# Kernel optimization log

Hardware: AMD Instinct MI355X
Metric: run time of the kernel (lower is better)

Reference implementation:

```python
import jax, jax.numpy as jnp
import numpy as np

B, N, F_IN, H, MH, STEPS = 8192, 9, 15, 128, 256, 4
E_PER = 16
MASK_IDX = jnp.arange(8)  # mask = [True]*8 + [False]


def setup_inputs() -> dict:
    key = jax.random.key(0)
    ks = jax.random.split(key, 24)
    s = 0.05
    inp = {
        "obs": jax.random.normal(ks[0], (B, 135), jnp.float32),
        "edges": jax.random.randint(ks[1], (B, 2, E_PER), 0, N, jnp.int32),
        "enc_W": jax.random.normal(ks[2], (F_IN, H), jnp.float32) * s,
        "enc_b": jax.random.normal(ks[3], (H,), jnp.float32) * s,
        "msg_W1": jax.random.normal(ks[4], (STEPS, 2 * H, MH), jnp.float32) * s,
        "msg_b1": jax.random.normal(ks[5], (STEPS, MH), jnp.float32) * s,
        "msg_W2": jax.random.normal(ks[6], (STEPS, MH, MH), jnp.float32) * s,
        "msg_b2": jax.random.normal(ks[7], (STEPS, MH), jnp.float32) * s,
        "msg_W3": jax.random.normal(ks[8], (STEPS, MH, H), jnp.float32) * s,
        "msg_b3": jax.random.normal(ks[9], (STEPS, H), jnp.float32) * s,
        "gru_Wi": jax.random.normal(ks[10], (STEPS, H, 3 * H), jnp.float32) * s,
        "gru_Wh": jax.random.normal(ks[11], (STEPS, H, 3 * H), jnp.float32) * s,
        "gru_bi": jax.random.normal(ks[12], (STEPS, 3 * H), jnp.float32) * s,
        "gru_bh": jax.random.normal(ks[13], (STEPS, 3 * H), jnp.float32) * s,
        "dec_W1": jax.random.normal(ks[14], (H, MH), jnp.float32) * s,
        "dec_b1": jax.random.normal(ks[15], (MH,), jnp.float32) * s,
        "dec_W2": jax.random.normal(ks[16], (MH, MH), jnp.float32) * s,
        "dec_b2": jax.random.normal(ks[17], (MH,), jnp.float32) * s,
        "dec_W3": jax.random.normal(ks[18], (MH, 1), jnp.float32) * s,
        "dec_b3": jax.random.normal(ks[19], (1,), jnp.float32) * s,
    }
    return inp


def reference(obs, edges, enc_W, enc_b, msg_W1, msg_b1, msg_W2, msg_b2,
              msg_W3, msg_b3, gru_Wi, gru_Wh, gru_bi, gru_bh,
              dec_W1, dec_b1, dec_W2, dec_b2, dec_W3, dec_b3):
    BN = B * N
    x = obs.reshape(BN, F_IN)                       # [B*N, 15]
    x = jnp.tanh(x @ enc_W + enc_b)                 # encoder -> [B*N, H]

    # flatten per-graph edges into a global edge list, then add self-loops
    offsets = (jnp.arange(B, dtype=jnp.int32) * N)[:, None, None]
    eg = edges + offsets                            # [B, 2, 16]
    loops = jnp.arange(BN, dtype=jnp.int32)
    src = jnp.concatenate([eg[:, 0, :].reshape(-1), loops])  # x_j (source)
    dst = jnp.concatenate([eg[:, 1, :].reshape(-1), loops])  # x_i (target)
    deg = jax.ops.segment_sum(jnp.ones_like(dst, dtype=x.dtype), dst,
                              num_segments=BN)      # >=1 due to self-loops

    for s in range(STEPS):
        m = jnp.concatenate([x[dst], x[src]], axis=-1)       # [E, 2H]
        m = jnp.tanh(m @ msg_W1[s] + msg_b1[s])
        m = jnp.tanh(m @ msg_W2[s] + msg_b2[s])
        m = m @ msg_W3[s] + msg_b3[s]                        # [E, H]
        aggr = jax.ops.segment_sum(m, dst, num_segments=BN) / deg[:, None]
        # GRUCell(input=aggr, hidden=x), PyTorch gate order (r, z, n)
        gi = aggr @ gru_Wi[s] + gru_bi[s]
        gh = x @ gru_Wh[s] + gru_bh[s]
        ir, iz, inn = jnp.split(gi, 3, axis=-1)
        hr, hz, hn = jnp.split(gh, 3, axis=-1)
        r = jax.nn.sigmoid(ir + hr)
        z = jax.nn.sigmoid(iz + hz)
        n = jnp.tanh(inn + r * hn)
        x = (1.0 - z) * n + z * x

    d = jnp.tanh(x @ dec_W1 + dec_b1)
    d = jnp.tanh(d @ dec_W2 + dec_b2)
    d = d @ dec_W3 + dec_b3                                  # [B*N, 1]
    out = d.reshape(B, N)
    return out[:, MASK_IDX]                                  # [B, 8]
```

## Files before the change

kernel.cpp:

```cpp
#include <hip/hip_runtime.h>
#include <hip/hip_bf16.h>
#include <math.h>

#define BGR   8192
#define NND   9
#define BN    73728
#define NE    131072
#define H     128
#define MH    256
#define FIN   15

typedef __bf16 bf16_t;
typedef bf16_t bf16x8 __attribute__((ext_vector_type(8)));
typedef float  f32x4  __attribute__((ext_vector_type(4)));
typedef float  f32x16 __attribute__((ext_vector_type(16)));

__device__ __forceinline__ unsigned short f2bf(float f) {
    unsigned int u = __float_as_uint(f);
    u += 0x7fff + ((u >> 16) & 1);
    return (unsigned short)(u >> 16);
}
__device__ __forceinline__ unsigned int pkbf(float a, float b) {
    union { __hip_bfloat162 h; unsigned int u; } un;
    un.h = __float22bfloat162_rn(make_float2(a, b));
    return un.u;
}
__device__ __forceinline__ bf16x8 as_frag(int4 v) {
    union { int4 i; bf16x8 f; } u; u.i = v; return u.f;
}
__device__ __forceinline__ float fast_tanh(float v) {
    float e = __expf(2.0f * v);
    return 1.0f - __fdividef(2.0f, e + 1.0f);
}
__device__ __forceinline__ int sw16(int m, int k) {
    return m * 256 + ((((k >> 3) ^ (m & 15)) << 3) | (k & 7));
}
__device__ __forceinline__ int swp(int m, int k) {
    return m * 128 + ((((k >> 3) ^ (m & 15)) << 3) | (k & 7));
}
__device__ __forceinline__ int sw_off(int m, int k) {
    return m * 256 + ((((k >> 3) ^ (m & 7)) << 3) | (k & 7));
}

__global__ void deg_kernel(const int* __restrict__ edges, float* __restrict__ inv_deg) {
    int g = blockIdx.x * 256 + threadIdx.x;
    if (g >= BGR) return;
    int cnt[NND];
#pragma unroll
    for (int n = 0; n < NND; ++n) cnt[n] = 1;
    for (int j = 0; j < 16; ++j) {
        int d = edges[g * 32 + 16 + j];
#pragma unroll
        for (int n = 0; n < NND; ++n) cnt[n] += (d == n) ? 1 : 0;
    }
#pragma unroll
    for (int n = 0; n < NND; ++n) inv_deg[g * NND + n] = 1.0f / (float)cnt[n];
}

__global__ void enc_kernel(const float* __restrict__ obs, const float* __restrict__ W,
                           const float* __restrict__ b, float* __restrict__ x) {
    int tid = blockIdx.x * 256 + threadIdx.x;
    int i = tid >> 7, h = tid & 127;
    float acc = b[h];
#pragma unroll
    for (int k = 0; k < FIN; ++k) acc += obs[i * FIN + k] * W[k * H + h];
    x[i * H + h] = tanhf(acc);
}

__global__ void wt_kernel(const float* __restrict__ W1, const float* __restrict__ W2,
                          const float* __restrict__ W3, const float* __restrict__ Wi,
                          const float* __restrict__ Wh, const float* __restrict__ dW1,
                          const float* __restrict__ dW2, unsigned short* __restrict__ out) {
    int idx = blockIdx.x * 256 + threadIdx.x;
    float v;
    if (idx < 262144) {
        int s = idx >> 16, r = idx & 65535, n = r >> 8, k = r & 255;
        v = W1[(s << 16) + (k << 8) + n];
    } else if (idx < 524288) {
        int i2 = idx - 262144;
        int s = i2 >> 16, r = i2 & 65535, n = r >> 8, k = r & 255;
        v = W2[(s << 16) + (k << 8) + n];
    } else if (idx < 655360) {
        int i3 = idx - 524288;
        int s = i3 >> 15, r = i3 & 32767, n = r >> 8, k = r & 255;
        v = W3[(s << 15) + (k << 7) + n];
    } else if (idx < 1179648) {
        int i4 = idx - 655360;
        int s = i4 >> 17, rr = i4 & 131071;
        int p = rr >> 8, k = rr & 255;
        int w = p >> 6, rem = p & 63;
        int gate = rem >> 4, c = rem & 15;
        int h = w * 16 + c;
        const int sb = s * 49152;
        if (gate == 0)      v = (k < 128) ? Wi[sb + k * 384 + h]       : Wh[sb + (k - 128) * 384 + h];
        else if (gate == 1) v = (k < 128) ? Wi[sb + k * 384 + 128 + h] : Wh[sb + (k - 128) * 384 + 128 + h];
        else if (gate == 2) v = (k < 128) ? Wi[sb + k * 384 + 256 + h] : 0.f;
        else                v = (k < 128) ? 0.f                        : Wh[sb + (k - 128) * 384 + 256 + h];
    } else if (idx < 1212416) {
        int i5 = idx - 1179648;
        int n = i5 >> 7, k = i5 & 127;
        v = dW1[k * 256 + n];
    } else if (idx < 1277952) {
        int i6 = idx - 1212416;
        int n = i6 >> 8, k = i6 & 255;
        v = dW2[k * 256 + n];
    } else {
        int i7 = idx - 1277952;
        int s = i7 >> 16, rr = i7 & 65535;
        int p = rr >> 7, k = rr & 127;
        int w = p >> 6, rem = p & 63;
        int side = rem >> 5, c = rem & 31;
        int n = w * 32 + c;
        v = W1[(s << 16) + ((k + side * 128) << 8) + n];
    }
    out[idx] = f2bf(v);
}

__global__ __launch_bounds__(512, 4) void proj_mfma(
        const float* __restrict__ x, const unsigned short* __restrict__ W1P,
        const float* __restrict__ b1,
        const unsigned short* __restrict__ W2T, const float* __restrict__ b2,
        const unsigned short* __restrict__ W3T,
        unsigned short* __restrict__ P, float* __restrict__ aggr) {
    __shared__ unsigned short lbuf[64 * 128];
    __shared__ unsigned short abuf[64 * 256];
    const int t = threadIdx.x;
    const int n0 = blockIdx.x * 64;
    const int wv = t >> 6, ln = t & 63, l31 = ln & 31, lh = ln >> 5;

    {
        const int m = t >> 3, q = t & 7;
        const float* xs = x + (size_t)(n0 + m) * H + q * 16;
#pragma unroll
        for (int i = 0; i < 4; ++i) {
            float4 v = *(const float4*)(xs + i * 4);
            uint2 o; o.x = pkbf(v.x, v.y); o.y = pkbf(v.z, v.w);
            *(uint2*)(lbuf + swp(m, q * 16 + i * 4)) = o;
        }
    }
    __syncthreads();

    {
        f32x16 au[2], av[2];
#pragma unroll
        for (int a = 0; a < 2; ++a)
#pragma unroll
            for (int i = 0; i < 16; ++i) { au[a][i] = 0.f; av[a][i] = 0.f; }
        const unsigned short* wpu = W1P + (size_t)(wv * 64 + l31) * 128 + lh * 8;
        const unsigned short* wpv = W1P + (size_t)(wv * 64 + 32 + l31) * 128 + lh * 8;
#pragma unroll
        for (int ks = 0; ks < 8; ++ks) {
            const int kk = ks * 16 + lh * 8;
            bf16x8 a0 = as_frag(*(const int4*)(lbuf + swp(l31, kk)));
            bf16x8 a1 = as_frag(*(const int4*)(lbuf + swp(32 + l31, kk)));
            bf16x8 wu = as_frag(*(const int4*)(wpu + ks * 16));
            bf16x8 wvv = as_frag(*(const int4*)(wpv + ks * 16));
            au[0] = __builtin_amdgcn_mfma_f32_32x32x16_bf16(a0, wu, au[0], 0, 0, 0);
            au[1] = __builtin_amdgcn_mfma_f32_32x32x16_bf16(a1, wu, au[1], 0, 0, 0);
            av[0] = __builtin_amdgcn_mfma_f32_32x32x16_bf16(a0, wvv, av[0], 0, 0, 0);
            av[1] = __builtin_amdgcn_mfma_f32_32x32x16_bf16(a1, wvv, av[1], 0, 0, 0);
        }
        const int n = wv * 32 + l31;
        const float bias = b1[n];
#pragma unroll
        for (int mt = 0; mt < 2; ++mt)
#pragma unroll
            for (int reg = 0; reg < 16; ++reg) {
                const int mrow = mt * 32 + (reg & 3) + ((reg >> 2) << 3) + (lh << 2);
                const size_t node = n0 + mrow;
                P[node * 512 + n]       = f2bf(au[mt][reg]);
                P[node * 512 + 256 + n] = f2bf(av[mt][reg]);
                abuf[sw16(mrow, n)] = f2bf(fast_tanh(au[mt][reg] + av[mt][reg] + bias));
            }
    }
    __syncthreads();

    {
        f32x16 acc0, acc1;
#pragma unroll
        for (int i = 0; i < 16; ++i) { acc0[i] = 0.f; acc1[i] = 0.f; }
        const unsigned short* wp = W2T + (size_t)(wv * 32 + l31) * 256 + lh * 8;
#pragma unroll
        for (int ks = 0; ks < 16; ++ks) {
            const int kk = ks * 16 + lh * 8;
            bf16x8 a0 = as_frag(*(const int4*)(abuf + sw16(l31, kk)));
            bf16x8 a1 = as_frag(*(const int4*)(abuf + sw16(32 + l31, kk)));
            bf16x8 bw = as_frag(*(const int4*)(wp + ks * 16));
            acc0 = __builtin_amdgcn_mfma_f32_32x32x16_bf16(a0, bw, acc0, 0, 0, 0);
            acc1 = __builtin_amdgcn_mfma_f32_32x32x16_bf16(a1, bw, acc1, 0, 0, 0);
        }
        __syncthreads();
        const int n = wv * 32 + l31;
        const float bias = b2[n];
#pragma unroll
        for (int reg = 0; reg < 16; ++reg) {
            const int mrow = (reg & 3) + ((reg >> 2) << 3) + (lh << 2);
            abuf[sw16(mrow, n)]      = f2bf(fast_tanh(acc0[reg] + bias));
            abuf[sw16(32 + mrow, n)] = f2bf(fast_tanh(acc1[reg] + bias));
        }
    }
    __syncthreads();

    {
        const int mt = wv & 1, nq = wv >> 1;
        const int n = nq * 32 + l31;
        f32x16 acc;
#pragma unroll
        for (int i = 0; i < 16; ++i) acc[i] = 0.f;
        const unsigned short* wp = W3T + (size_t)n * 256 + lh * 8;
#pragma unroll
        for (int ks = 0; ks < 16; ++ks) {
            const int kk = ks * 16 + lh * 8;
            bf16x8 a = as_frag(*(const int4*)(abuf + sw16(mt * 32 + l31, kk)));
            bf16x8 bw = as_frag(*(const int4*)(wp + ks * 16));
            acc = __builtin_amdgcn_mfma_f32_32x32x16_bf16(a, bw, acc, 0, 0, 0);
        }
#pragma unroll
        for (int reg = 0; reg < 16; ++reg) {
            const int m = mt * 32 + (reg & 3) + ((reg >> 2) << 3) + (lh << 2);
            aggr[(size_t)(n0 + m) * H + n] = acc[reg];
        }
    }
}

__global__ __launch_bounds__(512, 4) void msg_mfma(
        const unsigned short* __restrict__ P, const int* __restrict__ edges,
        const float* __restrict__ b1,
        const unsigned short* __restrict__ W2T, const float* __restrict__ b2,
        const unsigned short* __restrict__ W3T,
        float* __restrict__ aggr) {
    __shared__ unsigned short bufA[64 * 256];
    __shared__ unsigned short bufB[64 * 256];
    __shared__ unsigned char sdstL[64];
    const int t  = threadIdx.x;
    const int e0 = blockIdx.x * 64;
    const int wv = t >> 6;
    const int ln = t & 63;
    const int l31 = ln & 31;
    const int lh  = ln >> 5;

    if (t < 64) {
        const int eg = e0 + t;
        sdstL[t] = (unsigned char)(((eg >> 4) & 3) * NND + edges[(eg >> 4) * 32 + 16 + (eg & 15)]);
    }
    {
        const int row = t >> 3;
        const int c0  = (t & 7) * 32;
        const int eg  = e0 + row;
        const int g = eg >> 4, j = eg & 15;
        const int sn = g * NND + edges[g * 32 + j];
        const int dn = g * NND + edges[g * 32 + 16 + j];
        const unsigned short* up = P + (size_t)dn * 512 + c0;
        const unsigned short* vp = P + (size_t)sn * 512 + 256 + c0;
#pragma unroll
        for (int i = 0; i < 4; ++i) {
            const uint4 uu = *(const uint4*)(up + i * 8);
            const uint4 vv = *(const uint4*)(vp + i * 8);
            const unsigned int ua[4] = {uu.x, uu.y, uu.z, uu.w};
            const unsigned int va[4] = {vv.x, vv.y, vv.z, vv.w};
            unsigned int op[4];
#pragma unroll
            for (int j2 = 0; j2 < 4; ++j2) {
                const float2 bb = *(const float2*)(b1 + c0 + i * 8 + j2 * 2);
                const float s0 = fast_tanh(__uint_as_float(ua[j2] << 16) +
                                           __uint_as_float(va[j2] << 16) + bb.x);
                const float s1 = fast_tanh(__uint_as_float(ua[j2] & 0xffff0000u) +
                                           __uint_as_float(va[j2] & 0xffff0000u) + bb.y);
                op[j2] = pkbf(s0, s1);
            }
            *(uint4*)(bufA + sw16(row, c0 + i * 8)) = make_uint4(op[0], op[1], op[2], op[3]);
        }
    }
    __syncthreads();

    {
        f32x16 acc0, acc1;
#pragma unroll
        for (int i = 0; i < 16; ++i) { acc0[i] = 0.f; acc1[i] = 0.f; }
        const unsigned short* wp = W2T + (size_t)(wv * 32 + l31) * 256 + lh * 8;
#pragma unroll
        for (int ks = 0; ks < 16; ++ks) {
            const int kk = ks * 16 + lh * 8;
            bf16x8 a0 = as_frag(*(const int4*)(bufA + sw16(l31, kk)));
            bf16x8 a1 = as_frag(*(const int4*)(bufA + sw16(32 + l31, kk)));
            bf16x8 bw = as_frag(*(const int4*)(wp + ks * 16));
            acc0 = __builtin_amdgcn_mfma_f32_32x32x16_bf16(a0, bw, acc0, 0, 0, 0);
            acc1 = __builtin_amdgcn_mfma_f32_32x32x16_bf16(a1, bw, acc1, 0, 0, 0);
        }
        const int n = wv * 32 + l31;
        const float bias = b2[n];
#pragma unroll
        for (int reg = 0; reg < 16; ++reg) {
            const int mrow = (reg & 3) + ((reg >> 2) << 3) + (lh << 2);
            bufB[sw16(mrow, n)]      = f2bf(fast_tanh(acc0[reg] + bias));
            bufB[sw16(32 + mrow, n)] = f2bf(fast_tanh(acc1[reg] + bias));
        }
    }
    __syncthreads();

    float* aL = (float*)bufA;
#pragma unroll
    for (int i = 0; i < 9; ++i) aL[i * 512 + t] = 0.f;
    __syncthreads();

    {
        const int mt = wv & 1, nq = wv >> 1;
        const int n = nq * 32 + l31;
        f32x16 acc;
#pragma unroll
        for (int i = 0; i < 16; ++i) acc[i] = 0.f;
        const unsigned short* wp = W3T + (size_t)n * 256 + lh * 8;
#pragma unroll
        for (int ks = 0; ks < 16; ++ks) {
            const int kk = ks * 16 + lh * 8;
            bf16x8 a = as_frag(*(const int4*)(bufB + sw16(mt * 32 + l31, kk)));
            bf16x8 bw = as_frag(*(const int4*)(wp + ks * 16));
            acc = __builtin_amdgcn_mfma_f32_32x32x16_bf16(a, bw, acc, 0, 0, 0);
        }
#pragma unroll
        for (int reg = 0; reg < 16; ++reg) {
            const int m = mt * 32 + (reg & 3) + ((reg >> 2) << 3) + (lh << 2);
            atomicAdd(&aL[(int)sdstL[m] * 128 + n], acc[reg]);
        }
    }
    __syncthreads();

    {
        float* gp = aggr + (size_t)blockIdx.x * 36 * 128;
#pragma unroll
        for (int i = 0; i < 9; ++i) {
            const int idx = i * 512 + t;
            gp[idx] += aL[idx];
        }
    }
}

__global__ __launch_bounds__(512, 4) void gru_mfma(
        float* __restrict__ x, float* __restrict__ aggr, const float* __restrict__ inv_deg,
        const unsigned short* __restrict__ WG, const float* __restrict__ b3m,
        const float* __restrict__ bi, const float* __restrict__ bh) {
    __shared__ unsigned short bufA[64 * 256];
    const int t = threadIdx.x;
    const int n0 = blockIdx.x * 64;
    const int wv = t >> 6, ln = t & 63, lrow = ln & 15, lq = ln >> 4;

    {
        const int m = t >> 3;
        const int q = t & 7;
        const int k0 = q * 32;
        const int node = n0 + m;
        if (q < 4) {
            const float scale = inv_deg[node];
            const float* src = aggr + (size_t)node * H + k0;
#pragma unroll
            for (int i = 0; i < 8; ++i) {
                float4 v = *(const float4*)(src + i * 4);
                const float4 bb = *(const float4*)(b3m + k0 + i * 4);
                v.x = v.x * scale + bb.x; v.y = v.y * scale + bb.y;
                v.z = v.z * scale + bb.z; v.w = v.w * scale + bb.w;
                uint2 o; o.x = pkbf(v.x, v.y); o.y = pkbf(v.z, v.w);
                *(uint2*)(bufA + sw_off(m, k0 + i * 4)) = o;
            }
        } else {
            const float* src = x + (size_t)node * H + (k0 - 128);
#pragma unroll
            for (int i = 0; i < 8; ++i) {
                float4 v = *(const float4*)(src + i * 4);
                uint2 o; o.x = pkbf(v.x, v.y); o.y = pkbf(v.z, v.w);
                *(uint2*)(bufA + sw_off(m, k0 + i * 4)) = o;
            }
        }
    }
    __syncthreads();

    const f32x4 zero = {0.f, 0.f, 0.f, 0.f};
    f32x4 acc[4][4];
#pragma unroll
    for (int i = 0; i < 4; ++i)
#pragma unroll
        for (int j = 0; j < 4; ++j) acc[i][j] = zero;

    const unsigned short* wgp = WG + (size_t)(wv * 64 + lrow) * 256;
#pragma unroll
    for (int kq = 0; kq < 8; ++kq) {
        const int ko = kq * 32 + lq * 8;
        bf16x8 af[4], bfr[4];
#pragma unroll
        for (int tm = 0; tm < 4; ++tm)
            af[tm] = as_frag(*(const int4*)(bufA + sw_off(tm * 16 + lrow, ko)));
#pragma unroll
        for (int g = 0; g < 4; ++g)
            bfr[g] = as_frag(*(const int4*)(wgp + (size_t)g * 16 * 256 + ko));
#pragma unroll
        for (int tm = 0; tm < 4; ++tm)
#pragma unroll
            for (int g = 0; g < 4; ++g)
                acc[tm][g] = __builtin_amdgcn_mfma_f32_16x16x32_bf16(af[tm], bfr[g], acc[tm][g], 0, 0, 0);
    }

    {
        const int h = wv * 16 + lrow;
        const float b_r = bi[h] + bh[h];
        const float b_z = bi[128 + h] + bh[128 + h];
        const float b_n = bi[256 + h];
        const float b_h = bh[256 + h];
#pragma unroll
        for (int tm = 0; tm < 4; ++tm) {
#pragma unroll
            for (int r = 0; r < 4; ++r) {
                const int node = n0 + tm * 16 + lq * 4 + r;
                const float irhr = acc[tm][0][r] + b_r;
                const float izhz = acc[tm][1][r] + b_z;
                const float inn  = acc[tm][2][r] + b_n;
                const float hn   = acc[tm][3][r] + b_h;
                const float rg = 1.f / (1.f + expf(-irhr));
                const float zg = 1.f / (1.f + expf(-izhz));
                const float ng = tanhf(inn + rg * hn);
                const float xo = x[(size_t)node * H + h];
                x[(size_t)node * H + h] = (1.f - zg) * ng + zg * xo;
            }
        }
    }
}

__global__ __launch_bounds__(256, 4) void dec_mfma(
        const float* __restrict__ x,
        const unsigned short* __restrict__ W1T, const float* __restrict__ b1,
        const unsigned short* __restrict__ W2T, const float* __restrict__ b2,
        const float* __restrict__ W3, const float* __restrict__ b3,
        float* __restrict__ out) {
    __shared__ unsigned short buf[64 * 256];
    const int t = threadIdx.x;
    const int id0 = blockIdx.x * 64;
    const int wv = t >> 6, ln = t & 63, lrow = ln & 15, lq = ln >> 4;
    const int nbase = wv * 64;

    {
        const int m = t >> 2, q = t & 3;
        const int id = id0 + m;
        const int node = (id >> 3) * NND + (id & 7);
        const float* src = x + (size_t)node * H + q * 32;
#pragma unroll
        for (int i = 0; i < 8; ++i) {
            float4 v = *(const float4*)(src + i * 4);
            uint2 o; o.x = pkbf(v.x, v.y); o.y = pkbf(v.z, v.w);
            *(uint2*)(buf + sw_off(m, q * 32 + i * 4)) = o;
        }
    }
    __syncthreads();

    const f32x4 zero = {0.f, 0.f, 0.f, 0.f};

    {
        f32x4 acc[4][4];
#pragma unroll
        for (int i = 0; i < 4; ++i)
#pragma unroll
            for (int j = 0; j < 4; ++j) acc[i][j] = zero;
#pragma unroll
        for (int kq = 0; kq < 4; ++kq) {
            const int ko = kq * 32 + lq * 8;
            bf16x8 af[4], bfr[4];
#pragma unroll
            for (int tm = 0; tm < 4; ++tm)
                af[tm] = as_frag(*(const int4*)(buf + sw_off(tm * 16 + lrow, ko)));
#pragma unroll
            for (int tn = 0; tn < 4; ++tn)
                bfr[tn] = as_frag(*(const int4*)(W1T + (size_t)(nbase + tn * 16 + lrow) * 128 + ko));
#pragma unroll
            for (int tm = 0; tm < 4; ++tm)
#pragma unroll
                for (int tn = 0; tn < 4; ++tn)
                    acc[tm][tn] = __builtin_amdgcn_mfma_f32_16x16x32_bf16(af[tm], bfr[tn], acc[tm][tn], 0, 0, 0);
        }
        __syncthreads();
#pragma unroll
        for (int tn = 0; tn < 4; ++tn) {
            const int n = nbase + tn * 16 + lrow;
            const float bias = b1[n];
#pragma unroll
            for (int tm = 0; tm < 4; ++tm)
#pragma unroll
                for (int r = 0; r < 4; ++r) {
                    const int m = tm * 16 + lq * 4 + r;
                    buf[sw_off(m, n)] = f2bf(fast_tanh(acc[tm][tn][r] + bias));
                }
        }
    }
    __syncthreads();

    {
        f32x4 acc[4][4];
#pragma unroll
        for (int i = 0; i < 4; ++i)
#pragma unroll
            for (int j = 0; j < 4; ++j) acc[i][j] = zero;
#pragma unroll
        for (int kq = 0; kq < 8; ++kq) {
            const int ko = kq * 32 + lq * 8;
            bf16x8 af[4], bfr[4];
#pragma unroll
            for (int tm = 0; tm < 4; ++tm)
                af[tm] = as_frag(*(const int4*)(buf + sw_off(tm * 16 + lrow, ko)));
#pragma unroll
            for (int tn = 0; tn < 4; ++tn)
                bfr[tn] = as_frag(*(const int4*)(W2T + (size_t)(nbase + tn * 16 + lrow) * 256 + ko));
#pragma unroll
            for (int tm = 0; tm < 4; ++tm)
#pragma unroll
                for (int tn = 0; tn < 4; ++tn)
                    acc[tm][tn] = __builtin_amdgcn_mfma_f32_16x16x32_bf16(af[tm], bfr[tn], acc[tm][tn], 0, 0, 0);
        }
        __syncthreads();
#pragma unroll
        for (int tn = 0; tn < 4; ++tn) {
            const int n = nbase + tn * 16 + lrow;
            const float bias = b2[n];
#pragma unroll
            for (int tm = 0; tm < 4; ++tm)
#pragma unroll
                for (int r = 0; r < 4; ++r) {
                    const int m = tm * 16 + lq * 4 + r;
                    buf[sw_off(m, n)] = f2bf(fast_tanh(acc[tm][tn][r] + bias));
                }
        }
    }
    __syncthreads();

    {
        const int m = t >> 2, p = t & 3;
        float s = 0.f;
#pragma unroll
        for (int i = 0; i < 64; ++i) {
            const int k = p * 64 + i;
            const float a = __uint_as_float((unsigned int)buf[sw_off(m, k)] << 16);
            s += a * W3[k];
        }
        s += __shfl_xor(s, 1);
        s += __shfl_xor(s, 2);
        if (p == 0) out[id0 + m] = s + b3[0];
    }
}

extern "C" void kernel_launch(void* const* d_in, const int* in_sizes, int n_in,
                              void* d_out, int out_size, void* d_ws, size_t ws_size,
                              hipStream_t stream) {
    const float* obs    = (const float*)d_in[0];
    const int*   edges  = (const int*)  d_in[1];
    const float* enc_W  = (const float*)d_in[2];
    const float* enc_b  = (const float*)d_in[3];
    const float* msg_W1 = (const float*)d_in[4];
    const float* msg_b1 = (const float*)d_in[5];
    const float* msg_W2 = (const float*)d_in[6];
    const float* msg_b2 = (const float*)d_in[7];
    const float* msg_W3 = (const float*)d_in[8];
    const float* msg_b3 = (const float*)d_in[9];
    const float* gru_Wi = (const float*)d_in[10];
    const float* gru_Wh = (const float*)d_in[11];
    const float* gru_bi = (const float*)d_in[12];
    const float* gru_bh = (const float*)d_in[13];
    const float* dec_W1 = (const float*)d_in[14];
    const float* dec_b1 = (const float*)d_in[15];
    const float* dec_W2 = (const float*)d_in[16];
    const float* dec_b2 = (const float*)d_in[17];
    const float* dec_W3 = (const float*)d_in[18];
    const float* dec_b3 = (const float*)d_in[19];

    float* x       = (float*)d_ws;
    float* aggr    = x + (size_t)BN * H;
    float* inv_deg = aggr + (size_t)BN * H;
    unsigned short* wbf = (unsigned short*)(inv_deg + BN);
    unsigned short* P   = wbf + 1540096;

    deg_kernel<<<(BGR + 255) / 256, 256, 0, stream>>>(edges, inv_deg);
    wt_kernel<<<1540096 / 256, 256, 0, stream>>>(msg_W1, msg_W2, msg_W3, gru_Wi, gru_Wh,
                                                 dec_W1, dec_W2, wbf);
    enc_kernel<<<BN * H / 256, 256, 0, stream>>>(obs, enc_W, enc_b, x);

    for (int s = 0; s < 4; ++s) {
        const unsigned short* W2T = wbf + 262144 + (size_t)s * 65536;
        const unsigned short* W3T = wbf + 524288 + (size_t)s * 32768;
        const unsigned short* WGs = wbf + 655360 + (size_t)s * 131072;
        const unsigned short* W1P = wbf + 1277952 + (size_t)s * 65536;
        proj_mfma<<<BN / 64, 512, 0, stream>>>(
            x, W1P, msg_b1 + (size_t)s * 256,
            W2T, msg_b2 + (size_t)s * 256, W3T, P, aggr);
        msg_mfma<<<NE / 64, 512, 0, stream>>>(
            P, edges,
            msg_b1 + (size_t)s * 256,
            W2T, msg_b2 + (size_t)s * 256,
            W3T,
            aggr);
        gru_mfma<<<BN / 64, 512, 0, stream>>>(
            x, aggr, inv_deg, WGs, msg_b3 + (size_t)s * 128,
            gru_bi + (size_t)s * 384, gru_bh + (size_t)s * 384);
    }

    dec_mfma<<<BGR * 8 / 64, 256, 0, stream>>>(
        x, wbf + 1179648, dec_b1, wbf + 1212416, dec_b2, dec_W3, dec_b3, (float*)d_out);
}
```

Baseline: 1.499 ms.

## Fuse next-step node projection into GRU kernel to drop separate proj launches

The GRU kernel now also computes the next message-passing step's per-node projection: it keeps the updated node state as bf16 in shared memory and runs the W1/W2/W3 MLP chain, writing P and the self-loop aggregate. Only the first step still launches proj_mfma separately. This avoids re-reading x from global memory and removes three kernel launches. The cost is 16KB more shared memory per block and higher register pressure in the fused kernel, which may reduce occupancy.

```diff
diff --git a/kernel.cpp b/kernel.cpp
--- a/kernel.cpp
+++ b/kernel.cpp
@@ -335,14 +335,20 @@
     }
 }
 
-__global__ __launch_bounds__(512, 4) void gru_mfma(
+__global__ __launch_bounds__(512, 4) void grup_mfma(
         float* __restrict__ x, float* __restrict__ aggr, const float* __restrict__ inv_deg,
         const unsigned short* __restrict__ WG, const float* __restrict__ b3m,
-        const float* __restrict__ bi, const float* __restrict__ bh) {
+        const float* __restrict__ bi, const float* __restrict__ bh,
+        const unsigned short* __restrict__ W1Pn, const float* __restrict__ b1n,
+        const unsigned short* __restrict__ W2Tn, const float* __restrict__ b2n,
+        const unsigned short* __restrict__ W3Tn,
+        unsigned short* __restrict__ P, int do_next) {
     __shared__ unsigned short bufA[64 * 256];
+    __shared__ unsigned short xbL[64 * 128];
     const int t = threadIdx.x;
     const int n0 = blockIdx.x * 64;
     const int wv = t >> 6, ln = t & 63, lrow = ln & 15, lq = ln >> 4;
+    const int l31 = ln & 31, lh = ln >> 5;
 
     {
         const int m = t >> 3;
@@ -373,32 +379,32 @@
     }
     __syncthreads();
 
-    const f32x4 zero = {0.f, 0.f, 0.f, 0.f};
-    f32x4 acc[4][4];
-#pragma unroll
-    for (int i = 0; i < 4; ++i)
-#pragma unroll
-        for (int j = 0; j < 4; ++j) acc[i][j] = zero;
-
-    const unsigned short* wgp = WG + (size_t)(wv * 64 + lrow) * 256;
-#pragma unroll
-    for (int kq = 0; kq < 8; ++kq) {
-        const int ko = kq * 32 + lq * 8;
-        bf16x8 af[4], bfr[4];
-#pragma unroll
-        for (int tm = 0; tm < 4; ++tm)
-            af[tm] = as_frag(*(const int4*)(bufA + sw_off(tm * 16 + lrow, ko)));
-#pragma unroll
-        for (int g = 0; g < 4; ++g)
-            bfr[g] = as_frag(*(const int4*)(wgp + (size_t)g * 16 * 256 + ko));
-#pragma unroll
-        for (int tm = 0; tm < 4; ++tm)
+    {
+        const f32x4 zero = {0.f, 0.f, 0.f, 0.f};
+        f32x4 acc[4][4];
+#pragma unroll
+        for (int i = 0; i < 4; ++i)
+#pragma unroll
+            for (int j = 0; j < 4; ++j) acc[i][j] = zero;
+
+        const unsigned short* wgp = WG + (size_t)(wv * 64 + lrow) * 256;
+#pragma unroll
+        for (int kq = 0; kq < 8; ++kq) {
+            const int ko = kq * 32 + lq * 8;
+            bf16x8 af[4], bfr[4];
+#pragma unroll
+            for (int tm = 0; tm < 4; ++tm)
+                af[tm] = as_frag(*(const int4*)(bufA + sw_off(tm * 16 + lrow, ko)));
 #pragma unroll
             for (int g = 0; g < 4; ++g)
-                acc[tm][g] = __builtin_amdgcn_mfma_f32_16x16x32_bf16(af[tm], bfr[g], acc[tm][g], 0, 0, 0);
-    }
-
-    {
+                bfr[g] = as_frag(*(const int4*)(wgp + (size_t)g * 16 * 256 + ko));
+#pragma unroll
+            for (int tm = 0; tm < 4; ++tm)
+#pragma unroll
+                for (int g = 0; g < 4; ++g)
+                    acc[tm][g] = __builtin_amdgcn_mfma_f32_16x16x32_bf16(af[tm], bfr[g], acc[tm][g], 0, 0, 0);
+        }
+
         const int h = wv * 16 + lrow;
         const float b_r = bi[h] + bh[h];
         const float b_z = bi[128 + h] + bh[128 + h];
@@ -408,7 +414,8 @@
         for (int tm = 0; tm < 4; ++tm) {
 #pragma unroll
             for (int r = 0; r < 4; ++r) {
-                const int node = n0 + tm * 16 + lq * 4 + r;
+                const int ml = tm * 16 + lq * 4 + r;
+                const int node = n0 + ml;
                 const float irhr = acc[tm][0][r] + b_r;
                 const float izhz = acc[tm][1][r] + b_z;
                 const float inn  = acc[tm][2][r] + b_n;
@@ -417,8 +424,94 @@
                 const float zg = 1.f / (1.f + expf(-izhz));
                 const float ng = tanhf(inn + rg * hn);
                 const float xo = x[(size_t)node * H + h];
-                x[(size_t)node * H + h] = (1.f - zg) * ng + zg * xo;
+                const float xn = (1.f - zg) * ng + zg * xo;
+                x[(size_t)node * H + h] = xn;
+                xbL[swp(ml, h)] = f2bf(xn);
             }
+        }
+    }
+    if (!do_next) return;
+    __syncthreads();
+
+    {
+        f32x16 au[2], av[2];
+#pragma unroll
+        for (int a = 0; a < 2; ++a)
+#pragma unroll
+            for (int i = 0; i < 16; ++i) { au[a][i] = 0.f; av[a][i] = 0.f; }
+        const unsigned short* wpu = W1Pn + (size_t)(wv * 64 + l31) * 128 + lh * 8;
+        const unsigned short* wpv = W1Pn + (size_t)(wv * 64 + 32 + l31) * 128 + lh * 8;
+#pragma unroll
+        for (int ks = 0; ks < 8; ++ks) {
+            const int kk = ks * 16 + lh * 8;
+            bf16x8 a0 = as_frag(*(const int4*)(xbL + swp(l31, kk)));
+            bf16x8 a1 = as_frag(*(const int4*)(xbL + swp(32 + l31, kk)));
+            bf16x8 wu = as_frag(*(const int4*)(wpu + ks * 16));
+            bf16x8 wvv = as_frag(*(const int4*)(wpv + ks * 16));
+            au[0] = __builtin_amdgcn_mfma_f32_32x32x16_bf16(a0, wu, au[0], 0, 0, 0);
+            au[1] = __builtin_amdgcn_mfma_f32_32x32x16_bf16(a1, wu, au[1], 0, 0, 0);
+            av[0] = __builtin_amdgcn_mfma_f32_32x32x16_bf16(a0, wvv, av[0], 0, 0, 0);
+            av[1] = __builtin_amdgcn_mfma_f32_32x32x16_bf16(a1, wvv, av[1], 0, 0, 0);
+        }
+        const int n = wv * 32 + l31;
+        const float bias = b1n[n];
+#pragma unroll
+        for (int mt = 0; mt < 2; ++mt)
+#pragma unroll
+            for (int reg = 0; reg < 16; ++reg) {
+                const int mrow = mt * 32 + (reg & 3) + ((reg >> 2) << 3) + (lh << 2);
+                const size_t node = n0 + mrow;
+                P[node * 512 + n]       = f2bf(au[mt][reg]);
+                P[node * 512 + 256 + n] = f2bf(av[mt][reg]);
+                bufA[sw16(mrow, n)] = f2bf(fast_tanh(au[mt][reg] + av[mt][reg] + bias));
+            }
+    }
+    __syncthreads();
+
+    {
+        f32x16 acc0, acc1;
+#pragma unroll
+        for (int i = 0; i < 16; ++i) { acc0[i] = 0.f; acc1[i] = 0.f; }
+        const unsigned short* wp = W2Tn + (size_t)(wv * 32 + l31) * 256 + lh * 8;
+#pragma unroll
+        for (int ks = 0; ks < 16; ++ks) {
+            const int kk = ks * 16 + lh * 8;
+            bf16x8 a0 = as_frag(*(const int4*)(bufA + sw16(l31, kk)));
+            bf16x8 a1 = as_frag(*(const int4*)(bufA + sw16(32 + l31, kk)));
+            bf16x8 bw = as_frag(*(const int4*)(wp + ks * 16));
+            acc0 = __builtin_amdgcn_mfma_f32_32x32x16_bf16(a0, bw, acc0, 0, 0, 0);
+            acc1 = __builtin_amdgcn_mfma_f32_32x32x16_bf16(a1, bw, acc1, 0, 0, 0);
+        }
+        __syncthreads();
+        const int n = wv * 32 + l31;
+        const float bias = b2n[n];
+#pragma unroll
+        for (int reg = 0; reg < 16; ++reg) {
+            const int mrow = (reg & 3) + ((reg >> 2) << 3) + (lh << 2);
+            bufA[sw16(mrow, n)]      = f2bf(fast_tanh(acc0[reg] + bias));
+            bufA[sw16(32 + mrow, n)] = f2bf(fast_tanh(acc1[reg] + bias));
+        }
+    }
+    __syncthreads();
+
+    {
+        const int mt = wv & 1, nq = wv >> 1;
+        const int n = nq * 32 + l31;
+        f32x16 acc;
+#pragma unroll
+        for (int i = 0; i < 16; ++i) acc[i] = 0.f;
+        const unsigned short* wp = W3Tn + (size_t)n * 256 + lh * 8;
+#pragma unroll
+        for (int ks = 0; ks < 16; ++ks) {
+            const int kk = ks * 16 + lh * 8;
+            bf16x8 a = as_frag(*(const int4*)(bufA + sw16(mt * 32 + l31, kk)));
+            bf16x8 bw = as_frag(*(const int4*)(wp + ks * 16));
+            acc = __builtin_amdgcn_mfma_f32_32x32x16_bf16(a, bw, acc, 0, 0, 0);
+        }
+#pragma unroll
+        for (int reg = 0; reg < 16; ++reg) {
+            const int m = mt * 32 + (reg & 3) + ((reg >> 2) << 3) + (lh << 2);
+            aggr[(size_t)(n0 + m) * H + n] = acc[reg];
         }
     }
 }
@@ -577,23 +670,31 @@
                                                  dec_W1, dec_W2, wbf);
     enc_kernel<<<BN * H / 256, 256, 0, stream>>>(obs, enc_W, enc_b, x);
 
+    proj_mfma<<<BN / 64, 512, 0, stream>>>(
+        x, wbf + 1277952, msg_b1,
+        wbf + 262144, msg_b2, wbf + 524288, P, aggr);
+
     for (int s = 0; s < 4; ++s) {
         const unsigned short* W2T = wbf + 262144 + (size_t)s * 65536;
         const unsigned short* W3T = wbf + 524288 + (size_t)s * 32768;
         const unsigned short* WGs = wbf + 655360 + (size_t)s * 131072;
-        const unsigned short* W1P = wbf + 1277952 + (size_t)s * 65536;
-        proj_mfma<<<BN / 64, 512, 0, stream>>>(
-            x, W1P, msg_b1 + (size_t)s * 256,
-            W2T, msg_b2 + (size_t)s * 256, W3T, P, aggr);
+        const int nx = (s < 3) ? s + 1 : s;
+        const unsigned short* W1Pn = wbf + 1277952 + (size_t)nx * 65536;
+        const unsigned short* W2Tn = wbf + 262144 + (size_t)nx * 65536;
+        const unsigned short* W3Tn = wbf + 524288 + (size_t)nx * 32768;
         msg_mfma<<<NE / 64, 512, 0, stream>>>(
             P, edges,
             msg_b1 + (size_t)s * 256,
             W2T, msg_b2 + (size_t)s * 256,
             W3T,
             aggr);
-        gru_mfma<<<BN / 64, 512, 0, stream>>>(
+        grup_mfma<<<BN / 64, 512, 0, stream>>>(
             x, aggr, inv_deg, WGs, msg_b3 + (size_t)s * 128,
-            gru_bi + (size_t)s * 384, gru_bh + (size_t)s * 384);
+            gru_bi + (size_t)s * 384, gru_bh + (size_t)s * 384,
+            W1Pn, msg_b1 + (size_t)nx * 256,
+            W2Tn, msg_b2 + (size_t)nx * 256,
+            W3Tn,
+            P, (s < 3) ? 1 : 0);
     }
 
     dec_mfma<<<BGR * 8 / 64, 256, 0, stream>>>(
```

Measured after the change: 1.471 ms. Within noise of the previous version (-1.9%).
